# Optimization experiments

Hardware: AMD Instinct MI355X
Metric: run time of the kernel (lower is better)

## Reference

```python
import jax, jax.numpy as jnp
import numpy as np

DIM = 16
BOND = 4
RANK = 512
N = 50000
E = 400000
F_IN = 16
EDGE_VARIABLE = 2


def setup_inputs() -> dict:
    key = jax.random.key(0)
    ks = iter(jax.random.split(key, 48))
    g = lambda shape, s=0.1: jax.random.normal(next(ks), shape, jnp.float32) * s
    inp = {
        "x": jax.random.normal(next(ks), (N, F_IN), jnp.float32),
        "node_type": jax.random.randint(next(ks), (N,), 0, 3),
        "edge_index": jax.random.randint(next(ks), (2, E), 0, N),
        "edge_attr": jax.random.uniform(next(ks), (E, BOND), dtype=jnp.float32),
        # lin0
        "W_lin0": g((F_IN, DIM)), "b_lin0": jnp.zeros((DIM,), jnp.float32),
        # NNConv: root weight + edge-conditioned weight MLP (4 -> 32 -> dim*dim)
        "W_root": g((DIM, DIM)), "b_conv": jnp.zeros((DIM,), jnp.float32),
        "W_e1": g((BOND, 32)), "b_e1": jnp.zeros((32,), jnp.float32),
        "W_e2": g((32, DIM * DIM)), "b_e2": jnp.zeros((DIM * DIM,), jnp.float32),
        # GRU (torch gate order r,z,n), weights stored torch-style [3*dim, dim]
        "W_ih": g((3 * DIM, DIM)), "b_ih": jnp.zeros((3 * DIM,), jnp.float32),
        "W_hh": g((3 * DIM, DIM)), "b_hh": jnp.zeros((3 * DIM,), jnp.float32),
        # projections
        "W_lin1": g((DIM, BOND)), "b_lin1": jnp.zeros((BOND,), jnp.float32),
        "W_up": g((BOND, DIM)), "b_up": jnp.zeros((DIM,), jnp.float32),
        "W_down": g((DIM, BOND)), "b_down": jnp.zeros((BOND,), jnp.float32),
        # FGNet low-rank factor modules (rank 512)
        "U_B": g((DIM, RANK)), "V_B": g((RANK, DIM)),
        "U_C": g((DIM, RANK)), "V_C": g((RANK, DIM)),
        "U_A": g((BOND, RANK)), "V_A": g((RANK, BOND)),
        # fusion weights
        "w_node": g((1, DIM)), "W_lin": g((DIM, DIM)), "b_lin": jnp.zeros((DIM,), jnp.float32),
        "w_edge": g((1, BOND)), "W_line": g((BOND, BOND)), "b_line": jnp.zeros((BOND,), jnp.float32),
    }
    return inp


def _forward(x, edge_attr, W_lin0, b_lin0, W_root, b_conv, W_e1, b_e1, W_e2, b_e2,
             W_ih, b_ih, W_hh, b_hh, W_lin1, b_lin1, W_up, b_up, W_down, b_down,
             U_B, V_B, U_C, V_C, U_A, V_A, w_node, W_lin, b_lin, w_edge, W_line, b_line,
             node_type, edge_index):
    src, dst = edge_index[0], edge_index[1]

    def nnconv(out):
        # per-edge weight matrices from edge features (edge-conditioned conv)
        he = jax.nn.relu(edge_attr @ W_e1 + b_e1)
        We = (he @ W_e2 + b_e2).reshape(E, DIM, DIM)          # [E, dim, dim]
        m = jnp.einsum('ed,edk->ek', out[src], We)             # gather-multiply
        agg = jax.ops.segment_sum(m, dst, num_segments=N)      # scatter-add
        deg = jax.ops.segment_sum(jnp.ones((E,), out.dtype), dst, num_segments=N)
        agg = agg / jnp.clip(deg, 1.0)[:, None]                # mean aggregation
        return out @ W_root + b_conv + agg

    def gru(inp, h):
        gi = inp @ W_ih.T + b_ih
        gh = h @ W_hh.T + b_hh
        i_r, i_z, i_n = jnp.split(gi, 3, axis=-1)
        h_r, h_z, h_n = jnp.split(gh, 3, axis=-1)
        r = jax.nn.sigmoid(i_r + h_r)
        z = jax.nn.sigmoid(i_z + h_z)
        n = jnp.tanh(i_n + r * h_n)
        return (1.0 - z) * n + z * h

    out = jax.nn.relu(x @ W_lin0 + b_lin0)                     # [N, dim]
    h = out
    for _ in range(3):
        m = jax.nn.relu(nnconv(out))
        h = gru(m, h)
        out = h

    out_edges = jax.nn.relu(out @ W_lin1 + b_lin1)             # [N, bond]

    # one outer message-passing round (k in range(1))
    ev_mask = (node_type == EDGE_VARIABLE)[:, None]
    out_edges_up = out_edges @ W_up + b_up                     # [N, dim]
    out_combine = jnp.where(ev_mask, out_edges_up, out)        # masked replace

    # factor-B message (low-rank FGNet) -> node-dim message + down-projected edge msg
    msg_B = jax.nn.relu((out_combine @ U_B) @ V_B)             # [N, dim]
    msg_to_edge_B = msg_B @ W_down + b_down                    # [N, bond]

    # factor-C message (low-rank FGNet)
    msg_C = jax.nn.relu((out_combine @ U_C) @ V_C)             # [N, dim]

    # factor-A / valence message on edge-type beliefs
    msg_to_edge_A = jax.nn.relu((out_edges @ U_A) @ V_A)       # [N, bond]

    all_msg = msg_B + msg_C                                    # sum over stacked msgs
    combine_edge_msg = msg_to_edge_A * msg_to_edge_B

    out = out + jax.nn.relu((w_node * all_msg) @ W_lin + b_lin)
    out_edges = out_edges + jax.nn.relu((w_edge * combine_edge_msg) @ W_line + b_line)

    return jax.nn.log_softmax(out_edges, axis=-1)              # [N, bond]


def reference(x, node_type, edge_index, edge_attr, W_lin0, b_lin0, W_root, b_conv,
              W_e1, b_e1, W_e2, b_e2, W_ih, b_ih, W_hh, b_hh, W_lin1, b_lin1,
              W_up, b_up, W_down, b_down, U_B, V_B, U_C, V_C, U_A, V_A,
              w_node, W_lin, b_lin, w_edge, W_line, b_line):
    return _forward(x, edge_attr, W_lin0, b_lin0, W_root, b_conv, W_e1, b_e1, W_e2, b_e2,
                    W_ih, b_ih, W_hh, b_hh, W_lin1, b_lin1, W_up, b_up, W_down, b_down,
                    U_B, V_B, U_C, V_C, U_A, V_A, w_node, W_lin, b_lin, w_edge, W_line, b_line,
                    node_type, edge_index)
```

## Files before the change

kernel.cpp:

```cpp
#include <hip/hip_runtime.h>
#include <hip/hip_bf16.h>
#include <math.h>

#define N_NODES 50000
#define N_EDGES 400000
#define DIM 16
#define BOND 4
#define NCHUNK 25000
#define EDGE_GRID 784
#define E_BLOCKS 1563
#define PRE_BASE (E_BLOCKS - 68)
#define SCAN_TILE 1024
#define SCAN_BLOCKS 49

typedef __attribute__((ext_vector_type(8))) short short8;
typedef __attribute__((ext_vector_type(4))) float f32x4;

__device__ __forceinline__ float bf16_to_f32(unsigned short v) {
  return __uint_as_float(((unsigned int)v) << 16);
}

__global__ __launch_bounds__(256) void setup_kernel(
    const float* __restrict__ x, const float* __restrict__ W_lin0,
    const float* __restrict__ b_lin0, const float* __restrict__ ea,
    const float* __restrict__ We1, const float* __restrict__ be1,
    const int* __restrict__ ei, const float* __restrict__ U_B,
    const float* __restrict__ V_B, const float* __restrict__ U_A,
    const float* __restrict__ V_A, float* __restrict__ out,
    unsigned int* __restrict__ he_buf, int* __restrict__ degI,
    float* __restrict__ M_B, float* __restrict__ M_A) {
  __shared__ float sW0[256];
  __shared__ float sb0[16];
  __shared__ float sW1[128];
  __shared__ float sb1[32];
  int t = threadIdx.x;
  sW0[t] = W_lin0[t];
  if (t < 16) sb0[t] = b_lin0[t];
  if (t < 128) sW1[t] = We1[t];
  if (t < 32) sb1[t] = be1[t];
  __syncthreads();

  int gid = blockIdx.x * 256 + t;

  if (gid < N_NODES) {
    float xr[16];
#pragma unroll
    for (int d = 0; d < 16; ++d) xr[d] = x[gid * 16 + d];
#pragma unroll
    for (int k = 0; k < 16; ++k) {
      float acc = sb0[k];
#pragma unroll
      for (int d = 0; d < 16; ++d) acc += xr[d] * sW0[d * 16 + k];
      out[gid * 16 + k] = fmaxf(acc, 0.f);
    }
  }

  if (gid < N_EDGES) {
    float4 v = ((const float4*)ea)[gid];
    float h[32];
#pragma unroll
    for (int k = 0; k < 32; ++k) {
      float a = sb1[k] + v.x * sW1[k] + v.y * sW1[32 + k] + v.z * sW1[64 + k] +
                v.w * sW1[96 + k];
      h[k] = fmaxf(a, 0.f);
    }
    unsigned int u[16];
#pragma unroll
    for (int p = 0; p < 2; ++p)
#pragma unroll
      for (int tt = 0; tt < 8; ++tt) {
        float2 pr;
        pr.x = h[4 * tt + p];
        pr.y = h[4 * tt + 2 + p];
        __hip_bfloat162 b = __float22bfloat162_rn(pr);
        u[p * 8 + tt] = *(unsigned int*)&b;
      }
    uint4* dst = (uint4*)(he_buf + (size_t)gid * 16);
#pragma unroll
    for (int qq = 0; qq < 4; ++qq)
      dst[qq] =
          make_uint4(u[4 * qq], u[4 * qq + 1], u[4 * qq + 2], u[4 * qq + 3]);
    atomicAdd(&degI[ei[N_EDGES + gid]], 1);
  }

  if (blockIdx.x >= PRE_BASE) {
    int w = (blockIdx.x - PRE_BASE) * 4 + (t >> 6);
    int lane = t & 63;
    float partial = 0.f;
    if (w < 256) {
      int i = w >> 4, j = w & 15;
#pragma unroll
      for (int r8 = 0; r8 < 8; ++r8) {
        int r = lane + 64 * r8;
        partial += U_B[i * 512 + r] * V_B[r * 16 + j];
      }
    } else if (w < 272) {
      int a = (w - 256) >> 2, b = (w - 256) & 3;
#pragma unroll
      for (int r8 = 0; r8 < 8; ++r8) {
        int r = lane + 64 * r8;
        partial += U_A[a * 512 + r] * V_A[r * 4 + b];
      }
    }
#pragma unroll
    for (int off = 32; off > 0; off >>= 1)
      partial += __shfl_down(partial, off);
    if (lane == 0) {
      if (w < 256) M_B[w] = partial;
      else if (w < 272) M_A[w - 256] = partial;
    }
  }
}

__global__ __launch_bounds__(256) void scan_kernel(
    const int* __restrict__ degI, int* ticket, int* st,
    int* __restrict__ row_off, int* __restrict__ cur) {
  __shared__ int sdata[256];
  __shared__ int s_tile;
  __shared__ int s_base;
  int t = threadIdx.x;
  if (t == 0) s_tile = atomicAdd(ticket, 1);
  __syncthreads();
  int tile = s_tile;
  int n0 = tile * SCAN_TILE + t * 4;

  int d0 = (n0 + 0 < N_NODES) ? degI[n0 + 0] : 0;
  int d1 = (n0 + 1 < N_NODES) ? degI[n0 + 1] : 0;
  int d2 = (n0 + 2 < N_NODES) ? degI[n0 + 2] : 0;
  int d3 = (n0 + 3 < N_NODES) ? degI[n0 + 3] : 0;
  int tsum = d0 + d1 + d2 + d3;
  sdata[t] = tsum;
  __syncthreads();
  for (int off = 1; off < 256; off <<= 1) {
    int v = (t >= off) ? sdata[t - off] : 0;
    __syncthreads();
    sdata[t] += v;
    __syncthreads();
  }
  int excl = sdata[t] - tsum;
  int agg = sdata[255];

  if (t == 0) {
    if (tile == 0) {
      atomicExch(&st[0], (agg << 2) | 2);
      s_base = 0;
    } else {
      atomicExch(&st[tile], (agg << 2) | 1);
      int run = 0, idx = tile - 1;
      while (true) {
        int w = atomicAdd(&st[idx], 0);
        int stt = w & 3;
        if (stt == 2) { run += (w >> 2); break; }
        if (stt == 1) { run += (w >> 2); --idx; }
      }
      atomicExch(&st[tile], ((run + agg) << 2) | 2);
      s_base = run;
    }
  }
  __syncthreads();

  int pre = s_base + excl;
  if (n0 + 0 < N_NODES) { row_off[n0 + 0] = pre; cur[n0 + 0] = pre; }
  pre += d0;
  if (n0 + 1 < N_NODES) { row_off[n0 + 1] = pre; cur[n0 + 1] = pre; }
  pre += d1;
  if (n0 + 2 < N_NODES) { row_off[n0 + 2] = pre; cur[n0 + 2] = pre; }
  pre += d2;
  if (n0 + 3 < N_NODES) { row_off[n0 + 3] = pre; cur[n0 + 3] = pre; }
  if (tile == SCAN_BLOCKS - 1 && t == 0) row_off[N_NODES] = N_EDGES;
}

__global__ __launch_bounds__(256) void slot_kernel(const int* __restrict__ ei,
                                                   int* __restrict__ cur,
                                                   int* __restrict__ slot) {
  int e = blockIdx.x * 256 + threadIdx.x;
  if (e < N_EDGES) slot[e] = atomicAdd(&cur[ei[N_EDGES + e]], 1);
}

__global__ __launch_bounds__(256) void edge_msg_mfma_kernel(
    const int* __restrict__ ei, const unsigned int* __restrict__ he_buf,
    const float* __restrict__ We2, const float* __restrict__ be2,
    const float* __restrict__ out, const int* __restrict__ slot,
    unsigned short* __restrict__ m_bufh) {
  const int lane = threadIdx.x & 63;
  const int q = lane >> 4, n = lane & 15;
  const int p = q >> 1, dbase = (q & 1) * 8;

  short8 bfrag[17];
#pragma unroll
  for (int s = 0; s < 16; ++s) {
    int h = 2 * s + p;
    union { short8 v; __hip_bfloat162 b2[4]; } bf;
#pragma unroll
    for (int jj = 0; jj < 4; ++jj) {
      float2 w;
      w.x = We2[h * 256 + (dbase + 2 * jj) * 16 + n];
      w.y = We2[h * 256 + (dbase + 2 * jj + 1) * 16 + n];
      bf.b2[jj] = __float22bfloat162_rn(w);
    }
    bfrag[s] = bf.v;
  }
  {
    union { short8 v; __hip_bfloat162 b2[4]; } bf;
#pragma unroll
    for (int jj = 0; jj < 4; ++jj) {
      float2 w;
      if (q < 2) {
        w.x = be2[(dbase + 2 * jj) * 16 + n];
        w.y = be2[(dbase + 2 * jj + 1) * 16 + n];
      } else {
        w.x = 0.f; w.y = 0.f;
      }
      bf.b2[jj] = __float22bfloat162_rn(w);
    }
    bfrag[16] = bf.v;
  }

  int wave = blockIdx.x * 4 + (threadIdx.x >> 6);
  const int nw = EDGE_GRID * 4;
  for (int c = wave; c < NCHUNK; c += nw) {
    int e = c * 16 + n;
    int src = ei[e];
    const uint4* hp = (const uint4*)(he_buf + (size_t)e * 16 + p * 8);
    uint4 h0 = hp[0], h1 = hp[1];
    unsigned int heu[8] = {h0.x, h0.y, h0.z, h0.w, h1.x, h1.y, h1.z, h1.w};
    const float4* op = (const float4*)(out + src * 16 + dbase);
    float4 o0 = op[0], o1 = op[1];
    float o[8] = {o0.x, o0.y, o0.z, o0.w, o1.x, o1.y, o1.z, o1.w};

    f32x4 acc = {0.f, 0.f, 0.f, 0.f};
#pragma unroll
    for (int s = 0; s < 16; ++s) {
      unsigned int hw = heu[s >> 1];
      float he_s = __uint_as_float((s & 1) ? (hw & 0xffff0000u) : (hw << 16));
      union { short8 v; __hip_bfloat162 b2[4]; } af;
#pragma unroll
      for (int jj = 0; jj < 4; ++jj) {
        float2 pr;
        pr.x = he_s * o[2 * jj];
        pr.y = he_s * o[2 * jj + 1];
        af.b2[jj] = __float22bfloat162_rn(pr);
      }
      acc = __builtin_amdgcn_mfma_f32_16x16x32_bf16(af.v, bfrag[s], acc, 0, 0, 0);
    }
    {
      union { short8 v; __hip_bfloat162 b2[4]; } af;
#pragma unroll
      for (int jj = 0; jj < 4; ++jj) {
        float2 pr;
        if (q < 2) { pr.x = o[2 * jj]; pr.y = o[2 * jj + 1]; }
        else { pr.x = 0.f; pr.y = 0.f; }
        af.b2[jj] = __float22bfloat162_rn(pr);
      }
      acc = __builtin_amdgcn_mfma_f32_16x16x32_bf16(af.v, bfrag[16], acc, 0, 0, 0);
    }

    int4 sl4 = *(const int4*)(slot + c * 16 + q * 4);
    __hip_bfloat16 b0 = __float2bfloat16(acc[0]);
    __hip_bfloat16 b1 = __float2bfloat16(acc[1]);
    __hip_bfloat16 b2 = __float2bfloat16(acc[2]);
    __hip_bfloat16 b3 = __float2bfloat16(acc[3]);
    m_bufh[(size_t)sl4.x * 16 + n] = *(unsigned short*)&b0;
    m_bufh[(size_t)sl4.y * 16 + n] = *(unsigned short*)&b1;
    m_bufh[(size_t)sl4.z * 16 + n] = *(unsigned short*)&b2;
    m_bufh[(size_t)sl4.w * 16 + n] = *(unsigned short*)&b3;
  }
}

__global__ __launch_bounds__(256) void gather_gru_kernel(
    const int* __restrict__ row_off, const unsigned short* __restrict__ m_bufh,
    const float* __restrict__ Wroot, const float* __restrict__ bconv,
    const float* __restrict__ Wih, const float* __restrict__ bih,
    const float* __restrict__ Whh, const float* __restrict__ bhh,
    float* __restrict__ out, int do_final, const int* __restrict__ node_type,
    const float* __restrict__ Wlin1, const float* __restrict__ blin1,
    const float* __restrict__ Wup, const float* __restrict__ bup,
    const float* __restrict__ Wdown, const float* __restrict__ bdown,
    const float* __restrict__ M_B, const float* __restrict__ M_A,
    const float* __restrict__ wedge, const float* __restrict__ Wline,
    const float* __restrict__ bline, float* __restrict__ res) {
  __shared__ float sWr[256];
  __shared__ float sWihT[768];
  __shared__ float sWhhT[768];
  __shared__ float sb[112];
  int t = threadIdx.x;
  int kk = t >> 4, dd = t & 15;
  sWr[t] = Wroot[t];
#pragma unroll
  for (int g = 0; g < 3; ++g) {
    sWihT[g * 256 + dd * 16 + kk] = Wih[g * 256 + t];
    sWhhT[g * 256 + dd * 16 + kk] = Whh[g * 256 + t];
  }
  if (t < 16) sb[t] = bconv[t];
  else if (t < 64) sb[t] = bih[t - 16];
  else if (t < 112) sb[t] = bhh[t - 64];
  __syncthreads();

  int n = blockIdx.x * 16 + (t >> 4);
  int k = t & 15;
  int s0 = row_off[n], s1 = row_off[n + 1];

  float aggk = 0.f;
  for (int j = s0; j < s1; ++j) aggk += bf16_to_f32(m_bufh[(size_t)j * 16 + k]);
  float sc = 1.f / fmaxf((float)(s1 - s0), 1.f);

  float hk = out[n * 16 + k];

  float mk = sb[k] + aggk * sc;
#pragma unroll
  for (int d = 0; d < 16; ++d) mk += __shfl(hk, d, 16) * sWr[d * 16 + k];
  mk = fmaxf(mk, 0.f);

  float gir = sb[16 + k], giz = sb[32 + k], gin = sb[48 + k];
  float ghr = sb[64 + k], ghz = sb[80 + k], ghn = sb[96 + k];
#pragma unroll
  for (int d = 0; d < 16; ++d) {
    float md = __shfl(mk, d, 16);
    float hd = __shfl(hk, d, 16);
    gir += md * sWihT[d * 16 + k];
    giz += md * sWihT[256 + d * 16 + k];
    gin += md * sWihT[512 + d * 16 + k];
    ghr += hd * sWhhT[d * 16 + k];
    ghz += hd * sWhhT[256 + d * 16 + k];
    ghn += hd * sWhhT[512 + d * 16 + k];
  }
  float r = 1.f / (1.f + __expf(-(gir + ghr)));
  float z = 1.f / (1.f + __expf(-(giz + ghz)));
  float xn = gin + r * ghn;
  float ng = 1.f - 2.f / (__expf(2.f * xn) + 1.f);
  float hnew = (1.f - z) * ng + z * hk;

  if (!do_final) {
    out[n * 16 + k] = hnew;
    return;
  }

  float p0 = hnew * Wlin1[k * 4 + 0];
  float p1 = hnew * Wlin1[k * 4 + 1];
  float p2 = hnew * Wlin1[k * 4 + 2];
  float p3 = hnew * Wlin1[k * 4 + 3];
#pragma unroll
  for (int msk = 1; msk < 16; msk <<= 1) {
    p0 += __shfl_xor(p0, msk, 16);
    p1 += __shfl_xor(p1, msk, 16);
    p2 += __shfl_xor(p2, msk, 16);
    p3 += __shfl_xor(p3, msk, 16);
  }
  float oe0 = fmaxf(p0 + blin1[0], 0.f);
  float oe1 = fmaxf(p1 + blin1[1], 0.f);
  float oe2 = fmaxf(p2 + blin1[2], 0.f);
  float oe3 = fmaxf(p3 + blin1[3], 0.f);

  bool ev = (node_type[n] == 2);
  float ock = ev ? (bup[k] + oe0 * Wup[k] + oe1 * Wup[16 + k] +
                    oe2 * Wup[32 + k] + oe3 * Wup[48 + k])
                 : hnew;

  float msgBk = 0.f;
#pragma unroll
  for (int d = 0; d < 16; ++d) msgBk += __shfl(ock, d, 16) * M_B[d * 16 + k];
  msgBk = fmaxf(msgBk, 0.f);

  float q0 = msgBk * Wdown[k * 4 + 0];
  float q1 = msgBk * Wdown[k * 4 + 1];
  float q2 = msgBk * Wdown[k * 4 + 2];
  float q3 = msgBk * Wdown[k * 4 + 3];
#pragma unroll
  for (int msk = 1; msk < 16; msk <<= 1) {
    q0 += __shfl_xor(q0, msk, 16);
    q1 += __shfl_xor(q1, msk, 16);
    q2 += __shfl_xor(q2, msk, 16);
    q3 += __shfl_xor(q3, msk, 16);
  }
  float mtb0 = q0 + bdown[0], mtb1 = q1 + bdown[1];
  float mtb2 = q2 + bdown[2], mtb3 = q3 + bdown[3];

  float mta0 = fmaxf(oe0 * M_A[0] + oe1 * M_A[4] + oe2 * M_A[8] + oe3 * M_A[12], 0.f);
  float mta1 = fmaxf(oe0 * M_A[1] + oe1 * M_A[5] + oe2 * M_A[9] + oe3 * M_A[13], 0.f);
  float mta2 = fmaxf(oe0 * M_A[2] + oe1 * M_A[6] + oe2 * M_A[10] + oe3 * M_A[14], 0.f);
  float mta3 = fmaxf(oe0 * M_A[3] + oe1 * M_A[7] + oe2 * M_A[11] + oe3 * M_A[15], 0.f);

  float c0 = wedge[0] * (mta0 * mtb0);
  float c1 = wedge[1] * (mta1 * mtb1);
  float c2 = wedge[2] * (mta2 * mtb2);
  float c3 = wedge[3] * (mta3 * mtb3);

  float f0 = oe0 + fmaxf(bline[0] + c0 * Wline[0] + c1 * Wline[4] +
                         c2 * Wline[8] + c3 * Wline[12], 0.f);
  float f1 = oe1 + fmaxf(bline[1] + c0 * Wline[1] + c1 * Wline[5] +
                         c2 * Wline[9] + c3 * Wline[13], 0.f);
  float f2 = oe2 + fmaxf(bline[2] + c0 * Wline[2] + c1 * Wline[6] +
                         c2 * Wline[10] + c3 * Wline[14], 0.f);
  float f3 = oe3 + fmaxf(bline[3] + c0 * Wline[3] + c1 * Wline[7] +
                         c2 * Wline[11] + c3 * Wline[15], 0.f);

  float mx = fmaxf(fmaxf(f0, f1), fmaxf(f2, f3));
  float se = __expf(f0 - mx) + __expf(f1 - mx) + __expf(f2 - mx) +
             __expf(f3 - mx);
  float lse = mx + __logf(se);
  if (k < 4) {
    float v = (k == 0) ? f0 : (k == 1) ? f1 : (k == 2) ? f2 : f3;
    res[n * 4 + k] = v - lse;
  }
}

extern "C" void kernel_launch(void* const* d_in, const int* in_sizes, int n_in,
                              void* d_out, int out_size, void* d_ws,
                              size_t ws_size, hipStream_t stream) {
  const float* x       = (const float*)d_in[0];
  const int* node_type = (const int*)d_in[1];
  const int* ei        = (const int*)d_in[2];
  const float* ea      = (const float*)d_in[3];
  const float* W_lin0  = (const float*)d_in[4];
  const float* b_lin0  = (const float*)d_in[5];
  const float* W_root  = (const float*)d_in[6];
  const float* b_conv  = (const float*)d_in[7];
  const float* W_e1    = (const float*)d_in[8];
  const float* b_e1    = (const float*)d_in[9];
  const float* W_e2    = (const float*)d_in[10];
  const float* b_e2    = (const float*)d_in[11];
  const float* W_ih    = (const float*)d_in[12];
  const float* b_ih    = (const float*)d_in[13];
  const float* W_hh    = (const float*)d_in[14];
  const float* b_hh    = (const float*)d_in[15];
  const float* W_lin1  = (const float*)d_in[16];
  const float* b_lin1  = (const float*)d_in[17];
  const float* W_up    = (const float*)d_in[18];
  const float* b_up    = (const float*)d_in[19];
  const float* W_down  = (const float*)d_in[20];
  const float* b_down  = (const float*)d_in[21];
  const float* U_B     = (const float*)d_in[22];
  const float* V_B     = (const float*)d_in[23];
  const float* U_A     = (const float*)d_in[26];
  const float* V_A     = (const float*)d_in[27];
  const float* w_edge  = (const float*)d_in[31];
  const float* W_line  = (const float*)d_in[32];
  const float* b_line  = (const float*)d_in[33];

  float* ws    = (float*)d_ws;
  float* out   = ws;
  unsigned int* he_buf = (unsigned int*)(out + N_NODES * 16);
  unsigned short* m_bufh =
      (unsigned short*)(he_buf + (size_t)N_EDGES * 16);
  float* M_B   = (float*)(m_bufh + (size_t)N_EDGES * 16);
  float* M_A   = M_B + 256;
  int* degI    = (int*)(M_A + 16);
  int* ticket  = degI + N_NODES;
  int* st      = ticket + 1;
  int* row_off = st + 63;
  int* cur     = row_off + N_NODES + 1;
  int* slot    = cur + N_NODES;

  hipMemsetAsync(degI, 0, (N_NODES + 64) * sizeof(int), stream);

  setup_kernel<<<E_BLOCKS, 256, 0, stream>>>(
      x, W_lin0, b_lin0, ea, W_e1, b_e1, ei, U_B, V_B, U_A, V_A, out, he_buf,
      degI, M_B, M_A);
  scan_kernel<<<SCAN_BLOCKS, 256, 0, stream>>>(degI, ticket, st, row_off, cur);
  slot_kernel<<<E_BLOCKS, 256, 0, stream>>>(ei, cur, slot);

  for (int it = 0; it < 3; ++it) {
    edge_msg_mfma_kernel<<<EDGE_GRID, 256, 0, stream>>>(ei, he_buf, W_e2, b_e2,
                                                        out, slot, m_bufh);
    gather_gru_kernel<<<N_NODES / 16, 256, 0, stream>>>(
        row_off, m_bufh, W_root, b_conv, W_ih, b_ih, W_hh, b_hh, out,
        (it == 2) ? 1 : 0, node_type, W_lin1, b_lin1, W_up, b_up, W_down,
        b_down, M_B, M_A, w_edge, W_line, b_line, (float*)d_out);
  }
}
```

Measured before the change: 344.8 us.

## Fuse edge message MFMA with gather-GRU per 16-node group using dst-sorted edges

Edges are now physically sorted by destination in the slot kernel, which also computes the edge MLP hidden features directly into sorted order. Each iteration then runs one kernel where a wave processes a group of 16 destination nodes. It computes the per-edge MFMA messages for those nodes' contiguous edges, accumulates them into shared memory with LDS atomics, and applies the GRU update in place. This removes the bf16 message buffer write and re-read and one launch per iteration, and node state is ping-ponged between two buffers. In exchange, load imbalance across node groups and shared-memory atomic contention are possible, and the per-group edge loop has partial tail chunks.

Result: slower. 390.7 us (+13.3%).

```diff
diff --git a/kernel.cpp b/kernel.cpp
--- a/kernel.cpp
+++ b/kernel.cpp
@@ -4,14 +4,12 @@
 
 #define N_NODES 50000
 #define N_EDGES 400000
-#define DIM 16
-#define BOND 4
-#define NCHUNK 25000
-#define EDGE_GRID 784
+#define N_GROUPS 3125
 #define E_BLOCKS 1563
 #define PRE_BASE (E_BLOCKS - 68)
 #define SCAN_TILE 1024
 #define SCAN_BLOCKS 49
+#define ITER_GRID 782
 
 typedef __attribute__((ext_vector_type(8))) short short8;
 typedef __attribute__((ext_vector_type(4))) float f32x4;
@@ -22,22 +20,16 @@
 
 __global__ __launch_bounds__(256) void setup_kernel(
     const float* __restrict__ x, const float* __restrict__ W_lin0,
-    const float* __restrict__ b_lin0, const float* __restrict__ ea,
-    const float* __restrict__ We1, const float* __restrict__ be1,
-    const int* __restrict__ ei, const float* __restrict__ U_B,
-    const float* __restrict__ V_B, const float* __restrict__ U_A,
-    const float* __restrict__ V_A, float* __restrict__ out,
-    unsigned int* __restrict__ he_buf, int* __restrict__ degI,
-    float* __restrict__ M_B, float* __restrict__ M_A) {
+    const float* __restrict__ b_lin0, const int* __restrict__ ei,
+    const float* __restrict__ U_B, const float* __restrict__ V_B,
+    const float* __restrict__ U_A, const float* __restrict__ V_A,
+    float* __restrict__ out, int* __restrict__ degI, float* __restrict__ M_B,
+    float* __restrict__ M_A) {
   __shared__ float sW0[256];
   __shared__ float sb0[16];
-  __shared__ float sW1[128];
-  __shared__ float sb1[32];
   int t = threadIdx.x;
   sW0[t] = W_lin0[t];
   if (t < 16) sb0[t] = b_lin0[t];
-  if (t < 128) sW1[t] = We1[t];
-  if (t < 32) sb1[t] = be1[t];
   __syncthreads();
 
   int gid = blockIdx.x * 256 + t;
@@ -55,33 +47,7 @@
     }
   }
 
-  if (gid < N_EDGES) {
-    float4 v = ((const float4*)ea)[gid];
-    float h[32];
-#pragma unroll
-    for (int k = 0; k < 32; ++k) {
-      float a = sb1[k] + v.x * sW1[k] + v.y * sW1[32 + k] + v.z * sW1[64 + k] +
-                v.w * sW1[96 + k];
-      h[k] = fmaxf(a, 0.f);
-    }
-    unsigned int u[16];
-#pragma unroll
-    for (int p = 0; p < 2; ++p)
-#pragma unroll
-      for (int tt = 0; tt < 8; ++tt) {
-        float2 pr;
-        pr.x = h[4 * tt + p];
-        pr.y = h[4 * tt + 2 + p];
-        __hip_bfloat162 b = __float22bfloat162_rn(pr);
-        u[p * 8 + tt] = *(unsigned int*)&b;
-      }
-    uint4* dst = (uint4*)(he_buf + (size_t)gid * 16);
-#pragma unroll
-    for (int qq = 0; qq < 4; ++qq)
-      dst[qq] =
-          make_uint4(u[4 * qq], u[4 * qq + 1], u[4 * qq + 2], u[4 * qq + 3]);
-    atomicAdd(&degI[ei[N_EDGES + gid]], 1);
-  }
+  if (gid < N_EDGES) atomicAdd(&degI[ei[N_EDGES + gid]], 1);
 
   if (blockIdx.x >= PRE_BASE) {
     int w = (blockIdx.x - PRE_BASE) * 4 + (t >> 6);
@@ -103,8 +69,7 @@
       }
     }
 #pragma unroll
-    for (int off = 32; off > 0; off >>= 1)
-      partial += __shfl_down(partial, off);
+    for (int off = 32; off > 0; off >>= 1) partial += __shfl_down(partial, off);
     if (lane == 0) {
       if (w < 256) M_B[w] = partial;
       else if (w < 272) M_A[w - 256] = partial;
@@ -170,21 +135,87 @@
   if (tile == SCAN_BLOCKS - 1 && t == 0) row_off[N_NODES] = N_EDGES;
 }
 
-__global__ __launch_bounds__(256) void slot_kernel(const int* __restrict__ ei,
-                                                   int* __restrict__ cur,
-                                                   int* __restrict__ slot) {
-  int e = blockIdx.x * 256 + threadIdx.x;
-  if (e < N_EDGES) slot[e] = atomicAdd(&cur[ei[N_EDGES + e]], 1);
-}
-
-__global__ __launch_bounds__(256) void edge_msg_mfma_kernel(
-    const int* __restrict__ ei, const unsigned int* __restrict__ he_buf,
-    const float* __restrict__ We2, const float* __restrict__ be2,
-    const float* __restrict__ out, const int* __restrict__ slot,
-    unsigned short* __restrict__ m_bufh) {
-  const int lane = threadIdx.x & 63;
-  const int q = lane >> 4, n = lane & 15;
+__global__ __launch_bounds__(256) void slot_kernel(
+    const int* __restrict__ ei, const float* __restrict__ ea,
+    const float* __restrict__ We1, const float* __restrict__ be1,
+    int* __restrict__ cur, int* __restrict__ src_sorted,
+    int* __restrict__ dst_sorted, unsigned int* __restrict__ he_sorted) {
+  __shared__ float sW[128];
+  __shared__ float sb[32];
+  int t = threadIdx.x;
+  if (t < 128) sW[t] = We1[t];
+  if (t < 32) sb[t] = be1[t];
+  __syncthreads();
+  int e = blockIdx.x * 256 + t;
+  if (e >= N_EDGES) return;
+  int dst = ei[N_EDGES + e];
+  int s = atomicAdd(&cur[dst], 1);
+  src_sorted[s] = ei[e];
+  dst_sorted[s] = dst;
+
+  float4 v = ((const float4*)ea)[e];
+  float h[32];
+#pragma unroll
+  for (int k = 0; k < 32; ++k) {
+    float a = sb[k] + v.x * sW[k] + v.y * sW[32 + k] + v.z * sW[64 + k] +
+              v.w * sW[96 + k];
+    h[k] = fmaxf(a, 0.f);
+  }
+  unsigned int u[16];
+#pragma unroll
+  for (int p = 0; p < 2; ++p)
+#pragma unroll
+    for (int tt = 0; tt < 8; ++tt) {
+      float2 pr;
+      pr.x = h[4 * tt + p];
+      pr.y = h[4 * tt + 2 + p];
+      __hip_bfloat162 b = __float22bfloat162_rn(pr);
+      u[p * 8 + tt] = *(unsigned int*)&b;
+    }
+  uint4* dstp = (uint4*)(he_sorted + (size_t)s * 16);
+#pragma unroll
+  for (int qq = 0; qq < 4; ++qq)
+    dstp[qq] = make_uint4(u[4 * qq], u[4 * qq + 1], u[4 * qq + 2], u[4 * qq + 3]);
+}
+
+__global__ __launch_bounds__(256) void iter_kernel(
+    const int* __restrict__ row_off, const int* __restrict__ src_sorted,
+    const int* __restrict__ dst_sorted,
+    const unsigned int* __restrict__ he_sorted, const float* __restrict__ We2,
+    const float* __restrict__ be2, const float* __restrict__ in,
+    float* __restrict__ outb, const float* __restrict__ Wroot,
+    const float* __restrict__ bconv, const float* __restrict__ Wih,
+    const float* __restrict__ bih, const float* __restrict__ Whh,
+    const float* __restrict__ bhh, int do_final,
+    const int* __restrict__ node_type, const float* __restrict__ Wlin1,
+    const float* __restrict__ blin1, const float* __restrict__ Wup,
+    const float* __restrict__ bup, const float* __restrict__ Wdown,
+    const float* __restrict__ bdown, const float* __restrict__ M_B,
+    const float* __restrict__ M_A, const float* __restrict__ wedge,
+    const float* __restrict__ Wline, const float* __restrict__ bline,
+    float* __restrict__ res) {
+  __shared__ float sWr[256], sWihT[768], sWhhT[768], sbg[112];
+  __shared__ float sAgg[4 * 256];
+
+  int t = threadIdx.x;
+  {
+    int kk = t >> 4, dd = t & 15;
+    sWr[t] = Wroot[t];
+#pragma unroll
+    for (int g = 0; g < 3; ++g) {
+      sWihT[g * 256 + dd * 16 + kk] = Wih[g * 256 + t];
+      sWhhT[g * 256 + dd * 16 + kk] = Whh[g * 256 + t];
+    }
+    if (t < 16) sbg[t] = bconv[t];
+    else if (t < 64) sbg[t] = bih[t - 16];
+    else if (t < 112) sbg[t] = bhh[t - 64];
+  }
+
+  const int wv = t >> 6;
+  const int lane = t & 63;
+  const int q = lane >> 4, nn = lane & 15;
   const int p = q >> 1, dbase = (q & 1) * 8;
+  const int g = blockIdx.x * 4 + wv;
 
   short8 bfrag[17];
 #pragma unroll
@@ -194,8 +225,8 @@
 #pragma unroll
     for (int jj = 0; jj < 4; ++jj) {
       float2 w;
-      w.x = We2[h * 256 + (dbase + 2 * jj) * 16 + n];
-      w.y = We2[h * 256 + (dbase + 2 * jj + 1) * 16 + n];
+      w.x = We2[h * 256 + (dbase + 2 * jj) * 16 + nn];
+      w.y = We2[h * 256 + (dbase + 2 * jj + 1) * 16 + nn];
       bf.b2[jj] = __float22bfloat162_rn(w);
     }
     bfrag[s] = bf.v;
@@ -206,8 +237,8 @@
     for (int jj = 0; jj < 4; ++jj) {
       float2 w;
       if (q < 2) {
-        w.x = be2[(dbase + 2 * jj) * 16 + n];
-        w.y = be2[(dbase + 2 * jj + 1) * 16 + n];
+        w.x = be2[(dbase + 2 * jj) * 16 + nn];
+        w.y = be2[(dbase + 2 * jj + 1) * 16 + nn];
       } else {
         w.x = 0.f; w.y = 0.f;
       }
@@ -216,191 +247,171 @@
     bfrag[16] = bf.v;
   }
 
-  int wave = blockIdx.x * 4 + (threadIdx.x >> 6);
-  const int nw = EDGE_GRID * 4;
-  for (int c = wave; c < NCHUNK; c += nw) {
-    int e = c * 16 + n;
-    int src = ei[e];
-    const uint4* hp = (const uint4*)(he_buf + (size_t)e * 16 + p * 8);
-    uint4 h0 = hp[0], h1 = hp[1];
-    unsigned int heu[8] = {h0.x, h0.y, h0.z, h0.w, h1.x, h1.y, h1.z, h1.w};
-    const float4* op = (const float4*)(out + src * 16 + dbase);
-    float4 o0 = op[0], o1 = op[1];
-    float o[8] = {o0.x, o0.y, o0.z, o0.w, o1.x, o1.y, o1.z, o1.w};
-
-    f32x4 acc = {0.f, 0.f, 0.f, 0.f};
-#pragma unroll
-    for (int s = 0; s < 16; ++s) {
-      unsigned int hw = heu[s >> 1];
-      float he_s = __uint_as_float((s & 1) ? (hw & 0xffff0000u) : (hw << 16));
-      union { short8 v; __hip_bfloat162 b2[4]; } af;
-#pragma unroll
-      for (int jj = 0; jj < 4; ++jj) {
-        float2 pr;
-        pr.x = he_s * o[2 * jj];
-        pr.y = he_s * o[2 * jj + 1];
-        af.b2[jj] = __float22bfloat162_rn(pr);
-      }
-      acc = __builtin_amdgcn_mfma_f32_16x16x32_bf16(af.v, bfrag[s], acc, 0, 0, 0);
-    }
-    {
-      union { short8 v; __hip_bfloat162 b2[4]; } af;
-#pragma unroll
-      for (int jj = 0; jj < 4; ++jj) {
-        float2 pr;
-        if (q < 2) { pr.x = o[2 * jj]; pr.y = o[2 * jj + 1]; }
-        else { pr.x = 0.f; pr.y = 0.f; }
-        af.b2[jj] = __float22bfloat162_rn(pr);
-      }
-      acc = __builtin_amdgcn_mfma_f32_16x16x32_bf16(af.v, bfrag[16], acc, 0, 0, 0);
-    }
-
-    int4 sl4 = *(const int4*)(slot + c * 16 + q * 4);
-    __hip_bfloat16 b0 = __float2bfloat16(acc[0]);
-    __hip_bfloat16 b1 = __float2bfloat16(acc[1]);
-    __hip_bfloat16 b2 = __float2bfloat16(acc[2]);
-    __hip_bfloat16 b3 = __float2bfloat16(acc[3]);
-    m_bufh[(size_t)sl4.x * 16 + n] = *(unsigned short*)&b0;
-    m_bufh[(size_t)sl4.y * 16 + n] = *(unsigned short*)&b1;
-    m_bufh[(size_t)sl4.z * 16 + n] = *(unsigned short*)&b2;
-    m_bufh[(size_t)sl4.w * 16 + n] = *(unsigned short*)&b3;
-  }
-}
-
-__global__ __launch_bounds__(256) void gather_gru_kernel(
-    const int* __restrict__ row_off, const unsigned short* __restrict__ m_bufh,
-    const float* __restrict__ Wroot, const float* __restrict__ bconv,
-    const float* __restrict__ Wih, const float* __restrict__ bih,
-    const float* __restrict__ Whh, const float* __restrict__ bhh,
-    float* __restrict__ out, int do_final, const int* __restrict__ node_type,
-    const float* __restrict__ Wlin1, const float* __restrict__ blin1,
-    const float* __restrict__ Wup, const float* __restrict__ bup,
-    const float* __restrict__ Wdown, const float* __restrict__ bdown,
-    const float* __restrict__ M_B, const float* __restrict__ M_A,
-    const float* __restrict__ wedge, const float* __restrict__ Wline,
-    const float* __restrict__ bline, float* __restrict__ res) {
-  __shared__ float sWr[256];
-  __shared__ float sWihT[768];
-  __shared__ float sWhhT[768];
-  __shared__ float sb[112];
-  int t = threadIdx.x;
-  int kk = t >> 4, dd = t & 15;
-  sWr[t] = Wroot[t];
-#pragma unroll
-  for (int g = 0; g < 3; ++g) {
-    sWihT[g * 256 + dd * 16 + kk] = Wih[g * 256 + t];
-    sWhhT[g * 256 + dd * 16 + kk] = Whh[g * 256 + t];
-  }
-  if (t < 16) sb[t] = bconv[t];
-  else if (t < 64) sb[t] = bih[t - 16];
-  else if (t < 112) sb[t] = bhh[t - 64];
-  __syncthreads();
-
-  int n = blockIdx.x * 16 + (t >> 4);
-  int k = t & 15;
-  int s0 = row_off[n], s1 = row_off[n + 1];
-
-  float aggk = 0.f;
-  for (int j = s0; j < s1; ++j) aggk += bf16_to_f32(m_bufh[(size_t)j * 16 + k]);
-  float sc = 1.f / fmaxf((float)(s1 - s0), 1.f);
-
-  float hk = out[n * 16 + k];
-
-  float mk = sb[k] + aggk * sc;
-#pragma unroll
-  for (int d = 0; d < 16; ++d) mk += __shfl(hk, d, 16) * sWr[d * 16 + k];
-  mk = fmaxf(mk, 0.f);
-
-  float gir = sb[16 + k], giz = sb[32 + k], gin = sb[48 + k];
-  float ghr = sb[64 + k], ghz = sb[80 + k], ghn = sb[96 + k];
-#pragma unroll
-  for (int d = 0; d < 16; ++d) {
-    float md = __shfl(mk, d, 16);
-    float hd = __shfl(hk, d, 16);
-    gir += md * sWihT[d * 16 + k];
-    giz += md * sWihT[256 + d * 16 + k];
-    gin += md * sWihT[512 + d * 16 + k];
-    ghr += hd * sWhhT[d * 16 + k];
-    ghz += hd * sWhhT[256 + d * 16 + k];
-    ghn += hd * sWhhT[512 + d * 16 + k];
-  }
-  float r = 1.f / (1.f + __expf(-(gir + ghr)));
-  float z = 1.f / (1.f + __expf(-(giz + ghz)));
-  float xn = gin + r * ghn;
-  float ng = 1.f - 2.f / (__expf(2.f * xn) + 1.f);
-  float hnew = (1.f - z) * ng + z * hk;
-
-  if (!do_final) {
-    out[n * 16 + k] = hnew;
-    return;
-  }
-
-  float p0 = hnew * Wlin1[k * 4 + 0];
-  float p1 = hnew * Wlin1[k * 4 + 1];
-  float p2 = hnew * Wlin1[k * 4 + 2];
-  float p3 = hnew * Wlin1[k * 4 + 3];
-#pragma unroll
-  for (int msk = 1; msk < 16; msk <<= 1) {
-    p0 += __shfl_xor(p0, msk, 16);
-    p1 += __shfl_xor(p1, msk, 16);
-    p2 += __shfl_xor(p2, msk, 16);
-    p3 += __shfl_xor(p3, msk, 16);
-  }
-  float oe0 = fmaxf(p0 + blin1[0], 0.f);
-  float oe1 = fmaxf(p1 + blin1[1], 0.f);
-  float oe2 = fmaxf(p2 + blin1[2], 0.f);
-  float oe3 = fmaxf(p3 + blin1[3], 0.f);
-
-  bool ev = (node_type[n] == 2);
-  float ock = ev ? (bup[k] + oe0 * Wup[k] + oe1 * Wup[16 + k] +
-                    oe2 * Wup[32 + k] + oe3 * Wup[48 + k])
-                 : hnew;
-
-  float msgBk = 0.f;
-#pragma unroll
-  for (int d = 0; d < 16; ++d) msgBk += __shfl(ock, d, 16) * M_B[d * 16 + k];
-  msgBk = fmaxf(msgBk, 0.f);
-
-  float q0 = msgBk * Wdown[k * 4 + 0];
-  float q1 = msgBk * Wdown[k * 4 + 1];
-  float q2 = msgBk * Wdown[k * 4 + 2];
-  float q3 = msgBk * Wdown[k * 4 + 3];
-#pragma unroll
-  for (int msk = 1; msk < 16; msk <<= 1) {
-    q0 += __shfl_xor(q0, msk, 16);
-    q1 += __shfl_xor(q1, msk, 16);
-    q2 += __shfl_xor(q2, msk, 16);
-    q3 += __shfl_xor(q3, msk, 16);
-  }
-  float mtb0 = q0 + bdown[0], mtb1 = q1 + bdown[1];
-  float mtb2 = q2 + bdown[2], mtb3 = q3 + bdown[3];
-
-  float mta0 = fmaxf(oe0 * M_A[0] + oe1 * M_A[4] + oe2 * M_A[8] + oe3 * M_A[12], 0.f);
-  float mta1 = fmaxf(oe0 * M_A[1] + oe1 * M_A[5] + oe2 * M_A[9] + oe3 * M_A[13], 0.f);
-  float mta2 = fmaxf(oe0 * M_A[2] + oe1 * M_A[6] + oe2 * M_A[10] + oe3 * M_A[14], 0.f);
-  float mta3 = fmaxf(oe0 * M_A[3] + oe1 * M_A[7] + oe2 * M_A[11] + oe3 * M_A[15], 0.f);
-
-  float c0 = wedge[0] * (mta0 * mtb0);
-  float c1 = wedge[1] * (mta1 * mtb1);
-  float c2 = wedge[2] * (mta2 * mtb2);
-  float c3 = wedge[3] * (mta3 * mtb3);
-
-  float f0 = oe0 + fmaxf(bline[0] + c0 * Wline[0] + c1 * Wline[4] +
-                         c2 * Wline[8] + c3 * Wline[12], 0.f);
-  float f1 = oe1 + fmaxf(bline[1] + c0 * Wline[1] + c1 * Wline[5] +
-                         c2 * Wline[9] + c3 * Wline[13], 0.f);
-  float f2 = oe2 + fmaxf(bline[2] + c0 * Wline[2] + c1 * Wline[6] +
-                         c2 * Wline[10] + c3 * Wline[14], 0.f);
-  float f3 = oe3 + fmaxf(bline[3] + c0 * Wline[3] + c1 * Wline[7] +
-                         c2 * Wline[11] + c3 * Wline[15], 0.f);
-
-  float mx = fmaxf(fmaxf(f0, f1), fmaxf(f2, f3));
-  float se = __expf(f0 - mx) + __expf(f1 - mx) + __expf(f2 - mx) +
-             __expf(f3 - mx);
-  float lse = mx + __logf(se);
-  if (k < 4) {
-    float v = (k == 0) ? f0 : (k == 1) ? f1 : (k == 2) ? f2 : f3;
-    res[n * 4 + k] = v - lse;
+  int s0 = 0, s1 = 0;
+  float* sa = &sAgg[wv * 256];
+  if (g < N_GROUPS) {
+    int n0 = g * 16;
+    s0 = row_off[n0];
+    s1 = row_off[n0 + 16];
+    sa[lane] = 0.f;
+    sa[lane + 64] = 0.f;
+    sa[lane + 128] = 0.f;
+    sa[lane + 192] = 0.f;
+
+    for (int j0 = s0; j0 < s1; j0 += 16) {
+      int ja = j0 + nn;
+      bool va = (ja < s1);
+      int src = va ? src_sorted[ja] : 0;
+      const uint4* hp = (const uint4*)(he_sorted + (size_t)ja * 16 + p * 8);
+      uint4 h0 = hp[0], h1 = hp[1];
+      unsigned int heu[8] = {h0.x, h0.y, h0.z, h0.w, h1.x, h1.y, h1.z, h1.w};
+      const float4* op = (const float4*)(in + src * 16 + dbase);
+      float4 o0 = op[0], o1 = op[1];
+      float o[8] = {o0.x, o0.y, o0.z, o0.w, o1.x, o1.y, o1.z, o1.w};
+
+      f32x4 acc = {0.f, 0.f, 0.f, 0.f};
+#pragma unroll
+      for (int s = 0; s < 16; ++s) {
+        unsigned int hw = heu[s >> 1];
+        float he_s = __uint_as_float((s & 1) ? (hw & 0xffff0000u) : (hw << 16));
+        union { short8 v; __hip_bfloat162 b2[4]; } af;
+#pragma unroll
+        for (int jj = 0; jj < 4; ++jj) {
+          float2 pr;
+          pr.x = he_s * o[2 * jj];
+          pr.y = he_s * o[2 * jj + 1];
+          af.b2[jj] = __float22bfloat162_rn(pr);
+        }
+        acc = __builtin_amdgcn_mfma_f32_16x16x32_bf16(af.v, bfrag[s], acc, 0, 0, 0);
+      }
+      {
+        union { short8 v; __hip_bfloat162 b2[4]; } af;
+#pragma unroll
+        for (int jj = 0; jj < 4; ++jj) {
+          float2 pr;
+          if (q < 2) { pr.x = o[2 * jj]; pr.y = o[2 * jj + 1]; }
+          else { pr.x = 0.f; pr.y = 0.f; }
+          af.b2[jj] = __float22bfloat162_rn(pr);
+        }
+        acc = __builtin_amdgcn_mfma_f32_16x16x32_bf16(af.v, bfrag[16], acc, 0, 0, 0);
+      }
+
+#pragma unroll
+      for (int r = 0; r < 4; ++r) {
+        int j = j0 + q * 4 + r;
+        if (j < s1) {
+          int loc = dst_sorted[j] - g * 16;
+          atomicAdd(&sa[loc * 16 + nn], acc[r]);
+        }
+      }
+    }
+  }
+  __syncthreads();
+
+  if (g >= N_GROUPS) return;
+
+#pragma unroll
+  for (int loop = 0; loop < 4; ++loop) {
+    int nl = loop * 4 + q;
+    int n = g * 16 + nl;
+    int k = nn;
+    float aggk = sa[nl * 16 + k];
+    int r0 = row_off[n], r1 = row_off[n + 1];
+    float sc = 1.f / fmaxf((float)(r1 - r0), 1.f);
+    float hk = in[n * 16 + k];
+
+    float mk = sbg[k] + aggk * sc;
+#pragma unroll
+    for (int d = 0; d < 16; ++d) mk += __shfl(hk, d, 16) * sWr[d * 16 + k];
+    mk = fmaxf(mk, 0.f);
+
+    float gir = sbg[16 + k], giz = sbg[32 + k], gin = sbg[48 + k];
+    float ghr = sbg[64 + k], ghz = sbg[80 + k], ghn = sbg[96 + k];
+#pragma unroll
+    for (int d = 0; d < 16; ++d) {
+      float md = __shfl(mk, d, 16);
+      float hd = __shfl(hk, d, 16);
+      gir += md * sWihT[d * 16 + k];
+      giz += md * sWihT[256 + d * 16 + k];
+      gin += md * sWihT[512 + d * 16 + k];
+      ghr += hd * sWhhT[d * 16 + k];
+      ghz += hd * sWhhT[256 + d * 16 + k];
+      ghn += hd * sWhhT[512 + d * 16 + k];
+    }
+    float r = 1.f / (1.f + __expf(-(gir + ghr)));
+    float z = 1.f / (1.f + __expf(-(giz + ghz)));
+    float xn = gin + r * ghn;
+    float ng = 1.f - 2.f / (__expf(2.f * xn) + 1.f);
+    float hnew = (1.f - z) * ng + z * hk;
+
+    if (!do_final) {
+      outb[n * 16 + k] = hnew;
+      continue;
+    }
+
+    float p0 = hnew * Wlin1[k * 4 + 0];
+    float p1 = hnew * Wlin1[k * 4 + 1];
+    float p2 = hnew * Wlin1[k * 4 + 2];
+    float p3 = hnew * Wlin1[k * 4 + 3];
+#pragma unroll
+    for (int msk = 1; msk < 16; msk <<= 1) {
+      p0 += __shfl_xor(p0, msk, 16);
+      p1 += __shfl_xor(p1, msk, 16);
+      p2 += __shfl_xor(p2, msk, 16);
+      p3 += __shfl_xor(p3, msk, 16);
+    }
+    float oe0 = fmaxf(p0 + blin1[0], 0.f);
+    float oe1 = fmaxf(p1 + blin1[1], 0.f);
+    float oe2 = fmaxf(p2 + blin1[2], 0.f);
+    float oe3 = fmaxf(p3 + blin1[3], 0.f);
+
+    bool ev = (node_type[n] == 2);
+    float ock = ev ? (bup[k] + oe0 * Wup[k] + oe1 * Wup[16 + k] +
+                      oe2 * Wup[32 + k] + oe3 * Wup[48 + k])
+                   : hnew;
+
+    float msgBk = 0.f;
+#pragma unroll
+    for (int d = 0; d < 16; ++d) msgBk += __shfl(ock, d, 16) * M_B[d * 16 + k];
+    msgBk = fmaxf(msgBk, 0.f);
+
+    float q0 = msgBk * Wdown[k * 4 + 0];
+    float q1 = msgBk * Wdown[k * 4 + 1];
+    float q2 = msgBk * Wdown[k * 4 + 2];
+    float q3 = msgBk * Wdown[k * 4 + 3];
+#pragma unroll
+    for (int msk = 1; msk < 16; msk <<= 1) {
+      q0 += __shfl_xor(q0, msk, 16);
+      q1 += __shfl_xor(q1, msk, 16);
+      q2 += __shfl_xor(q2, msk, 16);
+      q3 += __shfl_xor(q3, msk, 16);
+    }
+    float mtb0 = q0 + bdown[0], mtb1 = q1 + bdown[1];
+    float mtb2 = q2 + bdown[2], mtb3 = q3 + bdown[3];
+
+    float mta0 = fmaxf(oe0 * M_A[0] + oe1 * M_A[4] + oe2 * M_A[8] + oe3 * M_A[12], 0.f);
+    float mta1 = fmaxf(oe0 * M_A[1] + oe1 * M_A[5] + oe2 * M_A[9] + oe3 * M_A[13], 0.f);
+    float mta2 = fmaxf(oe0 * M_A[2] + oe1 * M_A[6] + oe2 * M_A[10] + oe3 * M_A[14], 0.f);
+    float mta3 = fmaxf(oe0 * M_A[3] + oe1 * M_A[7] + oe2 * M_A[11] + oe3 * M_A[15], 0.f);
+
+    float c0 = wedge[0] * (mta0 * mtb0);
+    float c1 = wedge[1] * (mta1 * mtb1);
+    float c2 = wedge[2] * (mta2 * mtb2);
+    float c3 = wedge[3] * (mta3 * mtb3);
+
+    float f0 = oe0 + fmaxf(bline[0] + c0 * Wline[0] + c1 * Wline[4] + c2 * Wline[8] + c3 * Wline[12], 0.f);
+    float f1 = oe1 + fmaxf(bline[1] + c0 * Wline[1] + c1 * Wline[5] + c2 * Wline[9] + c3 * Wline[13], 0.f);
+    float f2 = oe2 + fmaxf(bline[2] + c0 * Wline[2] + c1 * Wline[6] + c2 * Wline[10] + c3 * Wline[14], 0.f);
+    float f3 = oe3 + fmaxf(bline[3] + c0 * Wline[3] + c1 * Wline[7] + c2 * Wline[11] + c3 * Wline[15], 0.f);
+
+    float mx = fmaxf(fmaxf(f0, f1), fmaxf(f2, f3));
+    float se = __expf(f0 - mx) + __expf(f1 - mx) + __expf(f2 - mx) +
+               __expf(f3 - mx);
+    float lse = mx + __logf(se);
+    if (k < 4) {
+      float v = (k == 0) ? f0 : (k == 1) ? f1 : (k == 2) ? f2 : f3;
+      res[n * 4 + k] = v - lse;
+    }
   }
 }
 
@@ -437,33 +448,33 @@
   const float* W_line  = (const float*)d_in[32];
   const float* b_line  = (const float*)d_in[33];
 
-  float* ws    = (float*)d_ws;
-  float* out   = ws;
-  unsigned int* he_buf = (unsigned int*)(out + N_NODES * 16);
-  unsigned short* m_bufh =
-      (unsigned short*)(he_buf + (size_t)N_EDGES * 16);
-  float* M_B   = (float*)(m_bufh + (size_t)N_EDGES * 16);
-  float* M_A   = M_B + 256;
-  int* degI    = (int*)(M_A + 16);
-  int* ticket  = degI + N_NODES;
-  int* st      = ticket + 1;
+  float* ws = (float*)d_ws;
+  float* out0 = ws;
+  float* out1 = out0 + N_NODES * 16;
+  unsigned int* he_sorted = (unsigned int*)(out1 + N_NODES * 16);
+  int* src_sorted = (int*)(he_sorted + (size_t)(N_EDGES + 16) * 16);
+  int* dst_sorted = src_sorted + N_EDGES + 16;
+  float* M_B = (float*)(dst_sorted + N_EDGES + 16);
+  float* M_A = M_B + 256;
+  int* degI = (int*)(M_A + 16);
+  int* ticket = degI + N_NODES;
+  int* st = ticket + 1;
   int* row_off = st + 63;
-  int* cur     = row_off + N_NODES + 1;
-  int* slot    = cur + N_NODES;
+  int* cur = row_off + N_NODES + 1;
 
   hipMemsetAsync(degI, 0, (N_NODES + 64) * sizeof(int), stream);
 
-  setup_kernel<<<E_BLOCKS, 256, 0, stream>>>(
-      x, W_lin0, b_lin0, ea, W_e1, b_e1, ei, U_B, V_B, U_A, V_A, out, he_buf,
-      degI, M_B, M_A);
+  setup_kernel<<<E_BLOCKS, 256, 0, stream>>>(x, W_lin0, b_lin0, ei, U_B, V_B,
+                                             U_A, V_A, out0, degI, M_B, M_A);
   scan_kernel<<<SCAN_BLOCKS, 256, 0, stream>>>(degI, ticket, st, row_off, cur);
-  slot_kernel<<<E_BLOCKS, 256, 0, stream>>>(ei, cur, slot);
-
+  slot_kernel<<<E_BLOCKS, 256, 0, stream>>>(ei, ea, W_e1, b_e1, cur, src_sorted,
+                                            dst_sorted, he_sorted);
+
+  float* bufs[2] = {out0, out1};
   for (int it = 0; it < 3; ++it) {
-    edge_msg_mfma_kernel<<<EDGE_GRID, 256, 0, stream>>>(ei, he_buf, W_e2, b_e2,
-                                                        out, slot, m_bufh);
-    gather_gru_kernel<<<N_NODES / 16, 256, 0, stream>>>(
-        row_off, m_bufh, W_root, b_conv, W_ih, b_ih, W_hh, b_hh, out,
+    iter_kernel<<<ITER_GRID, 256, 0, stream>>>(
+        row_off, src_sorted, dst_sorted, he_sorted, W_e2, b_e2, bufs[it & 1],
+        bufs[(it & 1) ^ 1], W_root, b_conv, W_ih, b_ih, W_hh, b_hh,
         (it == 2) ? 1 : 0, node_type, W_lin1, b_lin1, W_up, b_up, W_down,
         b_down, M_B, M_A, w_edge, W_line, b_line, (float*)d_out);
   }
```
